# Optimization experiments

Measured on AMD Instinct MI355X. Metric: run time of the kernel, lower is better.

Reference implementation:

```python
import jax, jax.numpy as jnp
import numpy as np

B, S, I, H, O, L = 64, 2048, 256, 256, 256, 2


def setup_inputs() -> dict:
    key = jax.random.key(0)
    ks = jax.random.split(key, 9)
    return {
        "x": jax.random.normal(ks[0], (B, S, I), dtype=jnp.float32),
        "w_h0": jax.random.normal(ks[1], (I, H), dtype=jnp.float32) * 0.05,
        "u_h0": jax.random.normal(ks[2], (H, H), dtype=jnp.float32) * 0.05,
        "b_h0": jax.random.uniform(ks[3], (H,), dtype=jnp.float32),
        "w_h1": jax.random.normal(ks[4], (H, H), dtype=jnp.float32) * 0.05,
        "u_h1": jax.random.normal(ks[5], (H, H), dtype=jnp.float32) * 0.05,
        "b_h1": jax.random.uniform(ks[6], (H,), dtype=jnp.float32),
        "w_q": jax.random.normal(ks[7], (H, O), dtype=jnp.float32) * 0.05,
        "b_q": jnp.zeros((O,), dtype=jnp.float32),
    }


def reference(x, w_h0, u_h0, b_h0, w_h1, u_h1, b_h1, w_q, b_q):
    batch = x.shape[0]
    h0_init = jnp.zeros((batch, H), dtype=x.dtype)
    h1_init = jnp.zeros((batch, H), dtype=x.dtype)

    def step(carry, x_t):
        h0, h1 = carry  # each [B, H]
        h0n = jnp.tanh(x_t @ w_h0 + h0 @ u_h0 + b_h0)
        h1n = jnp.tanh(h0n @ w_h1 + h1 @ u_h1 + b_h1)
        y = h1n @ w_q + b_q  # [B, O]
        return (h0n, h1n), y

    (h0_f, h1_f), ys = jax.lax.scan(step, (h0_init, h1_init),
                                    jnp.swapaxes(x, 0, 1))  # xs: [S, B, I]
    out = jnp.swapaxes(ys, 0, 1)  # [B, S, O]
    h_final = jnp.stack([h0_f, h1_f], axis=1)  # [B, L, H]
    return out, h_final
```

## Files before the change

### kernel.cpp

```cpp
#include <hip/hip_runtime.h>

#define S_LEN 2048
#define NB    64
#define HD    256

typedef _Float16 half2_t  __attribute__((ext_vector_type(2)));
typedef _Float16 half8_t  __attribute__((ext_vector_type(8)));
typedef float    floatx4  __attribute__((ext_vector_type(4)));
typedef float    floatx8  __attribute__((ext_vector_type(8)));
typedef float    floatx16 __attribute__((ext_vector_type(16)));

__device__ __forceinline__ float fdot2(half2_t a, half2_t b, float c){
#if __has_builtin(__builtin_amdgcn_fdot2)
  return __builtin_amdgcn_fdot2(a, b, c, false);
#else
  return c + (float)a[0]*(float)b[0] + (float)a[1]*(float)b[1];
#endif
}

__device__ __forceinline__ float tanh_fast(float x){
  float e = __expf(2.0f * x);
  return 1.0f - 2.0f / (e + 1.0f);
}

#define FOR32(M) M(0)M(1)M(2)M(3)M(4)M(5)M(6)M(7)M(8)M(9)M(10)M(11)M(12)M(13) \
                 M(14)M(15)M(16)M(17)M(18)M(19)M(20)M(21)M(22)M(23)M(24)M(25) \
                 M(26)M(27)M(28)M(29)M(30)M(31)

#define DECLW(i)  half8_t W##i;
#define LOADW(i)  W##i = *(const half8_t*)(wp + (i)*2048);

#define DOT_STEP(i)                                                            \
  { half8_t c_ = hs_[i];                                                       \
    a0_ = fdot2(__builtin_shufflevector(c_, c_, 0, 1),                         \
                __builtin_shufflevector(W##i, W##i, 0, 1), a0_);               \
    a1_ = fdot2(__builtin_shufflevector(c_, c_, 2, 3),                         \
                __builtin_shufflevector(W##i, W##i, 2, 3), a1_);               \
    a2_ = fdot2(__builtin_shufflevector(c_, c_, 4, 5),                         \
                __builtin_shufflevector(W##i, W##i, 4, 5), a2_);               \
    a3_ = fdot2(__builtin_shufflevector(c_, c_, 6, 7),                         \
                __builtin_shufflevector(W##i, W##i, 6, 7), a3_); }

#define MATVEC_W(HS, ACC)                                                      \
  { float a0_=0.f, a1_=0.f, a2_=0.f, a3_=0.f;                                  \
    const half8_t* hs_ = (HS);                                                 \
    FOR32(DOT_STEP)                                                            \
    ACC = (a0_ + a1_) + (a2_ + a3_); }

__attribute__((amdgpu_flat_work_group_size(768, 768)))
__attribute__((amdgpu_waves_per_eu(3, 3)))
__global__ void rnn_kernel(const _Float16* __restrict__ A0,
                           const _Float16* __restrict__ u0sw,
                           const _Float16* __restrict__ w1sw,
                           const _Float16* __restrict__ u1sw,
                           const float* __restrict__ b_h1,
                           _Float16* __restrict__ H1,
                           float* __restrict__ hfinal)
{
  const int b    = blockIdx.x;
  const int tid  = threadIdx.x;
  const int wave = tid >> 6;
  const int lane = tid & 63;
  const int group = wave >> 2;
  const int col   = ((wave & 3) << 6) | lane;

  __shared__ __align__(16) _Float16 h0buf[2][HD];
  __shared__ __align__(16) _Float16 h1buf[2][HD];
  __shared__ __align__(16) float    wpart[2][HD];

  if (tid < HD){
    h0buf[0][tid] = (_Float16)0.f; h0buf[1][tid] = (_Float16)0.f;
    h1buf[0][tid] = (_Float16)0.f; h1buf[1][tid] = (_Float16)0.f;
    wpart[0][tid] = 0.f;           wpart[1][tid] = 0.f;
  }

  const _Float16* Wsw = (group == 0) ? u0sw : (group == 1) ? u1sw : w1sw;
  const _Float16* wp  = Wsw + col * 8;
  FOR32(DECLW)
  FOR32(LOADW)

  const size_t base = (size_t)b * S_LEN * HD;
  const float bias = (group == 1) ? b_h1[col] : 0.f;

  _Float16 a0p0 = (_Float16)0.f, a0p1 = (_Float16)0.f;
  if (group == 0){
    a0p0 = A0[base + 0 * HD + col];
    a0p1 = A0[base + 1 * HD + col];
  }

  __syncthreads();

  for (int tau = 0; tau < S_LEN + 2; ++tau){
    if (group == 0){
      if (tau < S_LEN){
        float acc; MATVEC_W((const half8_t*)(&h0buf[(tau + 1) & 1][0]), acc);
        float h = tanh_fast(acc + (float)a0p0);
        h0buf[tau & 1][col] = (_Float16)h;
        if (tau == S_LEN - 1) hfinal[(b << 9) + col] = h;
        a0p0 = a0p1;
        if (tau + 2 < S_LEN) a0p1 = A0[base + (size_t)(tau + 2) * HD + col];
      }
    } else if (group == 2){
      const int t1 = tau - 1;
      if (t1 >= 0 && t1 < S_LEN){
        float acc; MATVEC_W((const half8_t*)(&h0buf[t1 & 1][0]), acc);
        wpart[t1 & 1][col] = acc;
      }
    } else {
      const int t = tau - 2;
      if (t >= 0){
        float acc; MATVEC_W((const half8_t*)(&h1buf[(t + 1) & 1][0]), acc);
        float h = tanh_fast(acc + wpart[t & 1][col] + bias);
        h1buf[t & 1][col] = (_Float16)h;
        H1[base + (size_t)t * HD + col] = (_Float16)h;
        if (t == S_LEN - 1) hfinal[(b << 9) + HD + col] = h;
      }
    }
    __syncthreads();
  }
}

__global__ void prep_kernel(const float* __restrict__ w0, const float* __restrict__ wq,
                            const float* __restrict__ u0, const float* __restrict__ w1,
                            const float* __restrict__ u1,
                            _Float16* __restrict__ B0, _Float16* __restrict__ Bq,
                            _Float16* __restrict__ U0, _Float16* __restrict__ W1,
                            _Float16* __restrict__ U1)
{
  int i = blockIdx.x * 256 + threadIdx.x;
  for (int idx = i; idx < 65536; idx += 64 * 256){
    int k = idx >> 8, n = idx & 255;
    int sw = (k >> 3) * 2048 + n * 8 + (k & 7);
    B0[sw] = (_Float16)w0[idx];
    Bq[sw] = (_Float16)wq[idx];
    U0[sw] = (_Float16)u0[idx];
    W1[sw] = (_Float16)w1[idx];
    U1[sw] = (_Float16)u1[idx];
  }
}

template<bool A_FP32, bool C_FP16>
__launch_bounds__(512)
__global__ void gemm256(const void* __restrict__ Ap,
                        const _Float16* __restrict__ Bsw,
                        const float* __restrict__ bias,
                        void* __restrict__ Cp)
{
  const int wave = threadIdx.x >> 6;
  const int lane = threadIdx.x & 63;
  const int r  = lane & 31;
  const int hf = lane >> 5;
  const size_t rowt = (size_t)blockIdx.x * 256 + (size_t)wave * 32;

  floatx16 acc[8];
  #pragma unroll
  for (int i = 0; i < 8; ++i)
    #pragma unroll
    for (int j = 0; j < 16; ++j) acc[i][j] = 0.f;

  const size_t arow = rowt + (size_t)r;
  #pragma unroll
  for (int ks = 0; ks < 16; ++ks){
    half8_t af;
    if (A_FP32){
      const float* A = (const float*)Ap;
      const floatx4* p = (const floatx4*)(A + arow * 256 + ks * 16 + hf * 8);
      floatx4 v0 = p[0], v1 = p[1];
      floatx8 v = __builtin_shufflevector(v0, v1, 0, 1, 2, 3, 4, 5, 6, 7);
      af = __builtin_convertvector(v, half8_t);
    } else {
      const _Float16* A = (const _Float16*)Ap;
      af = *(const half8_t*)(A + arow * 256 + ks * 16 + hf * 8);
    }
    #pragma unroll
    for (int ct = 0; ct < 8; ++ct){
      half8_t bf = *(const half8_t*)(Bsw + (size_t)(ks * 2 + hf) * 2048 + (ct * 32 + r) * 8);
      acc[ct] = __builtin_amdgcn_mfma_f32_32x32x16_f16(af, bf, acc[ct], 0, 0, 0);
    }
  }

  #pragma unroll
  for (int ct = 0; ct < 8; ++ct){
    const int col = ct * 32 + r;
    const float bc = bias[col];
    #pragma unroll
    for (int reg = 0; reg < 16; ++reg){
      const int rl = (reg & 3) + 8 * (reg >> 2) + 4 * hf;
      const size_t idx = (rowt + rl) * 256 + col;
      float v = acc[ct][reg] + bc;
      if (C_FP16) ((_Float16*)Cp)[idx] = (_Float16)v;
      else        ((float*)Cp)[idx]    = v;
    }
  }
}

extern "C" void kernel_launch(void* const* d_in, const int* in_sizes, int n_in,
                              void* d_out, int out_size, void* d_ws, size_t ws_size,
                              hipStream_t stream)
{
  (void)in_sizes; (void)n_in; (void)out_size;

  const float* x    = (const float*)d_in[0];
  const float* w_h0 = (const float*)d_in[1];
  const float* u_h0 = (const float*)d_in[2];
  const float* b_h0 = (const float*)d_in[3];
  const float* w_h1 = (const float*)d_in[4];
  const float* u_h1 = (const float*)d_in[5];
  const float* b_h1 = (const float*)d_in[6];
  const float* w_q  = (const float*)d_in[7];
  const float* b_q  = (const float*)d_in[8];

  const size_t MSH = (size_t)NB * S_LEN * HD;
  float* y    = (float*)d_out;
  float* hfin = y + MSH;

  _Float16* H1 = (_Float16*)d_ws;
  _Float16 *A0, *B0sw, *Bqsw, *U0sw, *W1sw, *U1sw;
  if (ws_size >= (MSH * 2 + 5 * 65536) * sizeof(_Float16)){
    A0   = H1 + MSH;
    B0sw = A0 + MSH;
  } else {
    A0   = (_Float16*)d_out;
    B0sw = H1 + MSH;
  }
  Bqsw = B0sw + 65536;
  U0sw = Bqsw + 65536;
  W1sw = U0sw + 65536;
  U1sw = W1sw + 65536;

  prep_kernel<<<dim3(64), dim3(256), 0, stream>>>(w_h0, w_q, u_h0, w_h1, u_h1,
                                                  B0sw, Bqsw, U0sw, W1sw, U1sw);
  gemm256<true, true><<<dim3(512), dim3(512), 0, stream>>>((const void*)x, B0sw, b_h0, (void*)A0);
  rnn_kernel<<<dim3(NB), dim3(768), 0, stream>>>(A0, U0sw, W1sw, U1sw, b_h1, H1, hfin);
  gemm256<false, false><<<dim3(512), dim3(512), 0, stream>>>((const void*)H1, Bqsw, b_q, (void*)y);
}
```

Before: 2.594 ms.

## Split fused two-layer RNN into per-layer recurrences with a batched input GEMM

The single wavefront kernel that ran both RNN layers at once is replaced by one recurrence kernel per layer. The layer-1 input projection (h0 @ w_h1 + b_h1) moves out of the sequential loop into a parallel MFMA GEMM between the two recurrences. Each recurrence kernel splits the 256-long dot product across two half-waves and combines the halves with a cross-lane shuffle, so each thread holds half the weights and there are fewer waves per block. The trade-off is that the serial chain of synchronized steps roughly doubles (two passes of 2048 steps instead of one pipelined pass), in exchange for cheaper individual steps.

After: 3.237 ms. 1.25x slower.

```diff
diff --git a/kernel.cpp b/kernel.cpp
--- a/kernel.cpp
+++ b/kernel.cpp
@@ -23,99 +23,66 @@
   return 1.0f - 2.0f / (e + 1.0f);
 }
 
-#define FOR32(M) M(0)M(1)M(2)M(3)M(4)M(5)M(6)M(7)M(8)M(9)M(10)M(11)M(12)M(13) \
-                 M(14)M(15)M(16)M(17)M(18)M(19)M(20)M(21)M(22)M(23)M(24)M(25) \
-                 M(26)M(27)M(28)M(29)M(30)M(31)
-
-#define DECLW(i)  half8_t W##i;
-#define LOADW(i)  W##i = *(const half8_t*)(wp + (i)*2048);
-
-#define DOT_STEP(i)                                                            \
-  { half8_t c_ = hs_[i];                                                       \
-    a0_ = fdot2(__builtin_shufflevector(c_, c_, 0, 1),                         \
-                __builtin_shufflevector(W##i, W##i, 0, 1), a0_);               \
-    a1_ = fdot2(__builtin_shufflevector(c_, c_, 2, 3),                         \
-                __builtin_shufflevector(W##i, W##i, 2, 3), a1_);               \
-    a2_ = fdot2(__builtin_shufflevector(c_, c_, 4, 5),                         \
-                __builtin_shufflevector(W##i, W##i, 4, 5), a2_);               \
-    a3_ = fdot2(__builtin_shufflevector(c_, c_, 6, 7),                         \
-                __builtin_shufflevector(W##i, W##i, 6, 7), a3_); }
-
-#define MATVEC_W(HS, ACC)                                                      \
-  { float a0_=0.f, a1_=0.f, a2_=0.f, a3_=0.f;                                  \
-    const half8_t* hs_ = (HS);                                                 \
-    FOR32(DOT_STEP)                                                            \
-    ACC = (a0_ + a1_) + (a2_ + a3_); }
-
-__attribute__((amdgpu_flat_work_group_size(768, 768)))
-__attribute__((amdgpu_waves_per_eu(3, 3)))
-__global__ void rnn_kernel(const _Float16* __restrict__ A0,
-                           const _Float16* __restrict__ u0sw,
-                           const _Float16* __restrict__ w1sw,
-                           const _Float16* __restrict__ u1sw,
-                           const float* __restrict__ b_h1,
-                           _Float16* __restrict__ H1,
-                           float* __restrict__ hfinal)
+#define SEL2(v,a,b) __builtin_shufflevector(v, v, a, b)
+#define FOR16(M) M(0)M(1)M(2)M(3)M(4)M(5)M(6)M(7)M(8)M(9)M(10)M(11)M(12)M(13)M(14)M(15)
+
+#define DECLW(i) half8_t W##i;
+#define LOADW(i) W##i = *(const half8_t*)(up + (i)*2048);
+
+#define DOTC(i) { half8_t c_ = hv[i];                                          \
+    a0 = fdot2(SEL2(c_,0,1), SEL2(W##i,0,1), a0);                              \
+    a1 = fdot2(SEL2(c_,2,3), SEL2(W##i,2,3), a1);                              \
+    a2 = fdot2(SEL2(c_,4,5), SEL2(W##i,4,5), a2);                              \
+    a3 = fdot2(SEL2(c_,6,7), SEL2(W##i,6,7), a3); }
+
+__attribute__((amdgpu_flat_work_group_size(512, 512)))
+__attribute__((amdgpu_waves_per_eu(2, 2)))
+__global__ void rnn_layer(const _Float16* __restrict__ A,
+                          const _Float16* __restrict__ Usw,
+                          _Float16* __restrict__ Hout,
+                          float* __restrict__ hfin_layer)
 {
   const int b    = blockIdx.x;
   const int tid  = threadIdx.x;
   const int wave = tid >> 6;
   const int lane = tid & 63;
-  const int group = wave >> 2;
-  const int col   = ((wave & 3) << 6) | lane;
-
-  __shared__ __align__(16) _Float16 h0buf[2][HD];
-  __shared__ __align__(16) _Float16 h1buf[2][HD];
-  __shared__ __align__(16) float    wpart[2][HD];
-
-  if (tid < HD){
-    h0buf[0][tid] = (_Float16)0.f; h0buf[1][tid] = (_Float16)0.f;
-    h1buf[0][tid] = (_Float16)0.f; h1buf[1][tid] = (_Float16)0.f;
-    wpart[0][tid] = 0.f;           wpart[1][tid] = 0.f;
-  }
-
-  const _Float16* Wsw = (group == 0) ? u0sw : (group == 1) ? u1sw : w1sw;
-  const _Float16* wp  = Wsw + col * 8;
-  FOR32(DECLW)
-  FOR32(LOADW)
+  const int c    = (wave << 5) | (lane & 31);
+  const int kh   = lane >> 5;
+
+  __shared__ __align__(16) _Float16 hbuf[2][HD];
+  if (tid < HD){ hbuf[0][tid] = (_Float16)0.f; hbuf[1][tid] = (_Float16)0.f; }
+
+  const _Float16* up = Usw + (size_t)(kh * 16) * 2048 + c * 8;
+  FOR16(DECLW)
+  FOR16(LOADW)
 
   const size_t base = (size_t)b * S_LEN * HD;
-  const float bias = (group == 1) ? b_h1[col] : 0.f;
-
-  _Float16 a0p0 = (_Float16)0.f, a0p1 = (_Float16)0.f;
-  if (group == 0){
-    a0p0 = A0[base + 0 * HD + col];
-    a0p1 = A0[base + 1 * HD + col];
-  }
+
+  _Float16 ap0 = A[base + 0 * HD + c];
+  _Float16 ap1 = A[base + 1 * HD + c];
 
   __syncthreads();
 
-  for (int tau = 0; tau < S_LEN + 2; ++tau){
-    if (group == 0){
-      if (tau < S_LEN){
-        float acc; MATVEC_W((const half8_t*)(&h0buf[(tau + 1) & 1][0]), acc);
-        float h = tanh_fast(acc + (float)a0p0);
-        h0buf[tau & 1][col] = (_Float16)h;
-        if (tau == S_LEN - 1) hfinal[(b << 9) + col] = h;
-        a0p0 = a0p1;
-        if (tau + 2 < S_LEN) a0p1 = A0[base + (size_t)(tau + 2) * HD + col];
-      }
-    } else if (group == 2){
-      const int t1 = tau - 1;
-      if (t1 >= 0 && t1 < S_LEN){
-        float acc; MATVEC_W((const half8_t*)(&h0buf[t1 & 1][0]), acc);
-        wpart[t1 & 1][col] = acc;
-      }
+  for (int t = 0; t < S_LEN; ++t){
+    const half8_t* hv = (const half8_t*)(&hbuf[t & 1][kh * 128]);
+
+    float a0=0.f, a1=0.f, a2=0.f, a3=0.f;
+    FOR16(DOTC)
+    float s = (a0 + a1) + (a2 + a3);
+    s += __shfl_xor(s, 32);
+
+    float h = tanh_fast(s + (float)ap0);
+    _Float16 hh = (_Float16)h;
+    if (kh == 0){
+      hbuf[(t + 1) & 1][c] = hh;
+      if (t == S_LEN - 1) hfin_layer[(b << 9) + c] = h;
     } else {
-      const int t = tau - 2;
-      if (t >= 0){
-        float acc; MATVEC_W((const half8_t*)(&h1buf[(t + 1) & 1][0]), acc);
-        float h = tanh_fast(acc + wpart[t & 1][col] + bias);
-        h1buf[t & 1][col] = (_Float16)h;
-        H1[base + (size_t)t * HD + col] = (_Float16)h;
-        if (t == S_LEN - 1) hfinal[(b << 9) + HD + col] = h;
-      }
-    }
+      Hout[base + (size_t)t * HD + c] = hh;
+    }
+
+    ap0 = ap1;
+    if (t + 2 < S_LEN) ap1 = A[base + (size_t)(t + 2) * HD + c];
+
     __syncthreads();
   }
 }
@@ -214,23 +181,25 @@
   float* y    = (float*)d_out;
   float* hfin = y + MSH;
 
-  _Float16* H1 = (_Float16*)d_ws;
-  _Float16 *A0, *B0sw, *Bqsw, *U0sw, *W1sw, *U1sw;
+  _Float16* bufH = (_Float16*)d_ws;
+  _Float16 *bufA, *B0sw;
   if (ws_size >= (MSH * 2 + 5 * 65536) * sizeof(_Float16)){
-    A0   = H1 + MSH;
-    B0sw = A0 + MSH;
+    bufA = bufH + MSH;
+    B0sw = bufA + MSH;
   } else {
-    A0   = (_Float16*)d_out;
-    B0sw = H1 + MSH;
-  }
-  Bqsw = B0sw + 65536;
-  U0sw = Bqsw + 65536;
-  W1sw = U0sw + 65536;
-  U1sw = W1sw + 65536;
+    bufA = (_Float16*)d_out;
+    B0sw = bufH + MSH;
+  }
+  _Float16* Bqsw = B0sw + 65536;
+  _Float16* U0sw = Bqsw + 65536;
+  _Float16* W1sw = U0sw + 65536;
+  _Float16* U1sw = W1sw + 65536;
 
   prep_kernel<<<dim3(64), dim3(256), 0, stream>>>(w_h0, w_q, u_h0, w_h1, u_h1,
                                                   B0sw, Bqsw, U0sw, W1sw, U1sw);
-  gemm256<true, true><<<dim3(512), dim3(512), 0, stream>>>((const void*)x, B0sw, b_h0, (void*)A0);
-  rnn_kernel<<<dim3(NB), dim3(768), 0, stream>>>(A0, U0sw, W1sw, U1sw, b_h1, H1, hfin);
-  gemm256<false, false><<<dim3(512), dim3(512), 0, stream>>>((const void*)H1, Bqsw, b_q, (void*)y);
-}
+  gemm256<true, true><<<dim3(512), dim3(512), 0, stream>>>((const void*)x, B0sw, b_h0, (void*)bufA);
+  rnn_layer<<<dim3(NB), dim3(512), 0, stream>>>(bufA, U0sw, bufH, hfin + 0);
+  gemm256<false, true><<<dim3(512), dim3(512), 0, stream>>>((const void*)bufH, W1sw, b_h1, (void*)bufA);
+  rnn_layer<<<dim3(NB), dim3(512), 0, stream>>>(bufA, U1sw, bufH, hfin + HD);
+  gemm256<false, false><<<dim3(512), dim3(512), 0, stream>>>((const void*)bufH, Bqsw, b_q, (void*)y);
+}
```
